# Optimization experiments

Hardware: AMD Instinct MI355X
Metric: run time of the kernel (lower is better)

## Reference

```python
import jax, jax.numpy as jnp
import numpy as np

DIM = 768
HEAD_DIM = 768


def setup_inputs() -> dict:
    key = jax.random.key(0)
    k_x, k_w, k_b = jax.random.split(key, 3)
    x = jax.random.normal(k_x, (4, 4096, DIM), dtype=jnp.float32)
    # torch Linear(dim, 3*head_dim): weight [3H, dim]; store transposed [dim, 3H]
    scale = 1.0 / np.sqrt(DIM)
    W_qkv = jax.random.uniform(k_w, (DIM, 3 * HEAD_DIM), dtype=jnp.float32,
                               minval=-scale, maxval=scale)
    b_qkv = jax.random.uniform(k_b, (3 * HEAD_DIM,), dtype=jnp.float32,
                               minval=-scale, maxval=scale)
    return {"x": x, "W_qkv": W_qkv, "b_qkv": b_qkv}


def reference(x, W_qkv, b_qkv):
    # x: [B, N, C]
    qkv = jnp.einsum("bnc,ch->bnh", x, W_qkv) + b_qkv  # [B, N, 3H]
    q, k, v = jnp.split(qkv, 3, axis=-1)               # each [B, N, H]
    H = q.shape[-1]
    scores = jnp.einsum("bnh,bmh->bnm", q, k) / jnp.sqrt(jnp.float32(H))
    attn = jax.nn.softmax(scores, axis=-1)             # [B, N, N]
    out = jnp.einsum("bnm,bmh->bnh", attn, v)          # [B, N, H]
    return out
```

## Files before the change

### kernel.cpp

```cpp
#include <hip/hip_runtime.h>
#include <stdint.h>

typedef __attribute__((ext_vector_type(8))) short short8;
typedef __attribute__((ext_vector_type(4))) float f32x4;

#define DIM 768
#define H3 2304
#define SEQ 4096
#define NTOK 16384

__device__ __forceinline__ unsigned short f2bf(float f) {
  union { float f; uint32_t u; } c; c.f = f;
  uint32_t u = c.u;
  u += 0x7FFFu + ((u >> 16) & 1u);
  return (unsigned short)(u >> 16);
}

__device__ __forceinline__ void async_cp16(const void* g, void* l) {
  __builtin_amdgcn_global_load_lds(
      (__attribute__((address_space(1))) void*)(void*)g,
      (__attribute__((address_space(3))) void*)l, 16, 0, 0);
}

#define MEMFENCE() asm volatile("" ::: "memory")
#define BARRIER() do { MEMFENCE(); __builtin_amdgcn_s_barrier(); MEMFENCE(); } while (0)
#define WAIT_LGK0() do { asm volatile("s_waitcnt lgkmcnt(0)" ::: "memory"); \
                         __builtin_amdgcn_sched_barrier(0); } while (0)
#define WAIT_VMCNT(n) asm volatile("s_waitcnt vmcnt(" #n ")" ::: "memory")

template<int JN>
__device__ __forceinline__ void gemm_nt64_t(
    const unsigned short* __restrict__ A, const unsigned short* __restrict__ B,
    int K, int ldA, int ldB,
    unsigned short* As, unsigned short* Bs, f32x4 acc[4][JN])
{
  const int tid = threadIdx.x, lane = tid & 63, wid = tid >> 6;
  const int wm = (wid & 1) << 6, wn = (wid >> 1) * (JN * 16);
  const int lr = lane & 15, q = lane >> 4;

#pragma unroll
  for (int i = 0; i < 4; ++i)
#pragma unroll
    for (int j = 0; j < JN; ++j)
      acc[i][j] = (f32x4){0.f, 0.f, 0.f, 0.f};

  const unsigned short* gA[4];
  const unsigned short* gB[JN];
#pragma unroll
  for (int t = 0; t < 4; ++t) {
    const int c = tid + 256 * t;
    const int row = c >> 3, sc = c & 7;
    gA[t] = A + (size_t)row * ldA + (((sc ^ (row & 7)) << 3));
  }
#pragma unroll
  for (int t = 0; t < JN; ++t) {
    const int c = tid + 256 * t;
    const int row = c >> 3, sc = c & 7;
    gB[t] = B + (size_t)row * ldB + (((sc ^ (row & 7)) << 3));
  }

  for (int k0 = 0; k0 < K; k0 += 64) {
#pragma unroll
    for (int t = 0; t < 4; ++t)
      async_cp16(gA[t] + k0, As + (tid + 256 * t) * 8);
#pragma unroll
    for (int t = 0; t < JN; ++t)
      async_cp16(gB[t] + k0, Bs + (tid + 256 * t) * 8);
    __syncthreads();

    short8 af[4][2], bfr[JN][2];
#pragma unroll
    for (int i = 0; i < 4; ++i) {
      const int ra = wm + i * 16 + lr;
#pragma unroll
      for (int s2 = 0; s2 < 2; ++s2)
        af[i][s2] = *(const short8*)(As + ra * 64 + (((s2 * 4 + q) ^ (ra & 7)) << 3));
    }
#pragma unroll
    for (int j = 0; j < JN; ++j) {
      const int rb = wn + j * 16 + lr;
#pragma unroll
      for (int s2 = 0; s2 < 2; ++s2)
        bfr[j][s2] = *(const short8*)(Bs + rb * 64 + (((s2 * 4 + q) ^ (rb & 7)) << 3));
    }
#pragma unroll
    for (int s2 = 0; s2 < 2; ++s2)
#pragma unroll
      for (int i = 0; i < 4; ++i)
#pragma unroll
        for (int j = 0; j < JN; ++j)
          acc[i][j] = __builtin_amdgcn_mfma_f32_16x16x32_bf16(af[i][s2], bfr[j][s2], acc[i][j], 0, 0, 0);
    __syncthreads();
  }
}

template<int JN>
__device__ __forceinline__ void gemm256_nt(
    const unsigned short* __restrict__ A, const unsigned short* __restrict__ B,
    int K, int ldA, int ldB, unsigned short* lds, f32x4 acc[8][JN])
{
  const int tid = threadIdx.x, lane = tid & 63, wid = tid >> 6;
  const int wr = wid >> 2, wc = wid & 3;
  const int lr = lane & 15, q = lane >> 4;

  unsigned short* const As0 = lds;
  unsigned short* const As1 = lds + 16384;
  unsigned short* const Bs0 = lds + 32768;
  unsigned short* const Bs1 = lds + 32768 + JN * 4096;

#pragma unroll
  for (int i = 0; i < 8; ++i)
#pragma unroll
    for (int j = 0; j < JN; ++j)
      acc[i][j] = (f32x4){0.f, 0.f, 0.f, 0.f};

  const unsigned short* gA[4];
  const unsigned short* gB[JN];
#pragma unroll
  for (int t = 0; t < 4; ++t) {
    const int c = tid + 512 * t, row = c >> 3, sc = c & 7;
    gA[t] = A + (size_t)row * ldA + ((sc ^ (row & 7)) << 3);
  }
#pragma unroll
  for (int t = 0; t < JN; ++t) {
    const int c = tid + 512 * t, row = c >> 3, sc = c & 7;
    gB[t] = B + (size_t)row * ldB + ((sc ^ (row & 7)) << 3);
  }

  const int nt = K >> 6;

#pragma unroll
  for (int t = 0; t < 4; ++t) async_cp16(gA[t], As0 + (tid + 512 * t) * 8);
#pragma unroll
  for (int t = 0; t < JN; ++t) async_cp16(gB[t], Bs0 + (tid + 512 * t) * 8);
  const int k1 = (nt > 1) ? 64 : 0;
#pragma unroll
  for (int t = 0; t < 4; ++t) async_cp16(gA[t] + k1, As1 + (tid + 512 * t) * 8);
  WAIT_VMCNT(4);
  BARRIER();

  short8 af[8], bf01[2], bfr[(JN > 2) ? (JN - 2) : 1];

#pragma unroll 2
  for (int t = 0; t < nt; ++t) {
    const int p = t & 1;
    const unsigned short* const Asp = p ? As1 : As0;
    const unsigned short* const Bsp = p ? Bs1 : Bs0;
    unsigned short* const Bsn = p ? Bs0 : Bs1;
    unsigned short* const Asn = p ? As1 : As0;
    const int kB = ((t + 1 < nt) ? t + 1 : nt - 1) << 6;
    const int kA = ((t + 2 < nt) ? t + 2 : nt - 1) << 6;

    async_cp16(gB[0] + kB, Bsn + tid * 8);
    async_cp16(gB[1] + kB, Bsn + (tid + 512) * 8);
#pragma unroll
    for (int i = 0; i < 8; ++i) {
      const int ra = wr * 128 + i * 16 + lr;
      af[i] = *(const short8*)(Asp + ra * 64 + ((q ^ (ra & 7)) << 3));
    }
#pragma unroll
    for (int j = 0; j < 2; ++j) {
      const int rb = wc * (JN * 16) + j * 16 + lr;
      bf01[j] = *(const short8*)(Bsp + rb * 64 + ((q ^ (rb & 7)) << 3));
    }
    BARRIER();
    WAIT_LGK0();
    __builtin_amdgcn_s_setprio(1);
#pragma unroll
    for (int i = 0; i < 8; ++i)
#pragma unroll
      for (int j = 0; j < 2; ++j)
        acc[i][j] = __builtin_amdgcn_mfma_f32_16x16x32_bf16(af[i], bf01[j], acc[i][j], 0, 0, 0);
    __builtin_amdgcn_s_setprio(0);
    BARRIER();

#pragma unroll
    for (int u = 2; u < JN; ++u)
      async_cp16(gB[u] + kB, Bsn + (tid + 512 * u) * 8);
#pragma unroll
    for (int j = 2; j < JN; ++j) {
      const int rb = wc * (JN * 16) + j * 16 + lr;
      bfr[j - 2] = *(const short8*)(Bsp + rb * 64 + ((q ^ (rb & 7)) << 3));
    }
    BARRIER();
    WAIT_LGK0();
    __builtin_amdgcn_s_setprio(1);
#pragma unroll
    for (int i = 0; i < 8; ++i)
#pragma unroll
      for (int j = 2; j < JN; ++j)
        acc[i][j] = __builtin_amdgcn_mfma_f32_16x16x32_bf16(af[i], bfr[j - 2], acc[i][j], 0, 0, 0);
    __builtin_amdgcn_s_setprio(0);
    BARRIER();

#pragma unroll
    for (int i = 0; i < 8; ++i) {
      const int ra = wr * 128 + i * 16 + lr;
      af[i] = *(const short8*)(Asp + ra * 64 + (((4 + q) ^ (ra & 7)) << 3));
    }
#pragma unroll
    for (int j = 0; j < 2; ++j) {
      const int rb = wc * (JN * 16) + j * 16 + lr;
      bf01[j] = *(const short8*)(Bsp + rb * 64 + (((4 + q) ^ (rb & 7)) << 3));
    }
    BARRIER();
    WAIT_LGK0();
    __builtin_amdgcn_s_setprio(1);
#pragma unroll
    for (int i = 0; i < 8; ++i)
#pragma unroll
      for (int j = 0; j < 2; ++j)
        acc[i][j] = __builtin_amdgcn_mfma_f32_16x16x32_bf16(af[i], bf01[j], acc[i][j], 0, 0, 0);
    __builtin_amdgcn_s_setprio(0);
    BARRIER();

#pragma unroll
    for (int u = 0; u < 4; ++u)
      async_cp16(gA[u] + kA, Asn + (tid + 512 * u) * 8);
#pragma unroll
    for (int j = 2; j < JN; ++j) {
      const int rb = wc * (JN * 16) + j * 16 + lr;
      bfr[j - 2] = *(const short8*)(Bsp + rb * 64 + (((4 + q) ^ (rb & 7)) << 3));
    }
    BARRIER();
    WAIT_LGK0();
    __builtin_amdgcn_s_setprio(1);
#pragma unroll
    for (int i = 0; i < 8; ++i)
#pragma unroll
      for (int j = 2; j < JN; ++j)
        acc[i][j] = __builtin_amdgcn_mfma_f32_16x16x32_bf16(af[i], bfr[j - 2], acc[i][j], 0, 0, 0);
    __builtin_amdgcn_s_setprio(0);
    WAIT_VMCNT(4);
    BARRIER();
  }
  WAIT_VMCNT(0);
  BARRIER();
}

__global__ __launch_bounds__(256) void k_cvt(const float* __restrict__ in,
                                             unsigned short* __restrict__ o) {
  int i = blockIdx.x * 256 + threadIdx.x;
  float4 f = ((const float4*)in)[i];
  ushort4 u;
  u.x = f2bf(f.x); u.y = f2bf(f.y); u.z = f2bf(f.z); u.w = f2bf(f.w);
  ((ushort4*)o)[i] = u;
}

__global__ __launch_bounds__(256) void k_transpose(const float* __restrict__ W,
                                                   unsigned short* __restrict__ Wt) {
  __shared__ float tile[32][33];
  const int bc = blockIdx.x * 32;
  const int br = blockIdx.y * 32;
  const int tx = threadIdx.x & 31, ty = threadIdx.x >> 5;
#pragma unroll
  for (int i = 0; i < 32; i += 8)
    tile[ty + i][tx] = W[(size_t)(br + ty + i) * H3 + bc + tx];
  __syncthreads();
#pragma unroll
  for (int i = 0; i < 32; i += 8)
    Wt[(size_t)(bc + ty + i) * DIM + br + tx] = f2bf(tile[tx][ty + i]);
}

__global__ __launch_bounds__(256) void k_qkv(
    const unsigned short* __restrict__ xbf, const unsigned short* __restrict__ Wt,
    const float* __restrict__ bias,
    unsigned short* __restrict__ qb, unsigned short* __restrict__ kb,
    unsigned short* __restrict__ vT)
{
  __shared__ unsigned short As[128 * 64];
  __shared__ unsigned short Bs[128 * 64];
  f32x4 acc[4][4];
  const int g = blockIdx.x;
  const int xcd = g & 7, slot = g >> 3;
  const int tn = slot % 18, grp = slot / 18;
  const int tm = xcd + 8 * grp;
  gemm_nt64_t<4>(xbf + (size_t)(tm * 128) * DIM, Wt + (size_t)(tn * 128) * DIM,
                 DIM, DIM, DIM, As, Bs, acc);

  const int tid = threadIdx.x, lane = tid & 63, wid = tid >> 6;
  const int wm = (wid & 1) << 6, wn = (wid >> 1) << 6;
  const float scale = 0.036084391824351615f;
#pragma unroll
  for (int i = 0; i < 4; ++i) {
#pragma unroll
    for (int j = 0; j < 4; ++j) {
      const int col  = tn * 128 + wn + j * 16 + (lane & 15);
      const int row0 = tm * 128 + wm + i * 16 + ((lane >> 4) << 2);
      const float bc = bias[col];
#pragma unroll
      for (int r = 0; r < 4; ++r) {
        const int row = row0 + r;
        const float v = acc[i][j][r] + bc;
        if (col < 768) {
          qb[(size_t)row * DIM + col] = f2bf(v * scale);
        } else if (col < 1536) {
          kb[(size_t)row * DIM + (col - 768)] = f2bf(v);
        } else {
          const int b = row >> 12, n = row & 4095;
          vT[((size_t)b * DIM + (col - 1536)) * SEQ + n] = f2bf(v);
        }
      }
    }
  }
}

__global__ __launch_bounds__(512, 2) void k_scores(
    const unsigned short* __restrict__ qb, const unsigned short* __restrict__ kb,
    unsigned short* __restrict__ S, float* __restrict__ lpart)
{
  __shared__ unsigned short lds[65536];
  f32x4 acc[8][4];
  const int g = blockIdx.x;
  const int xcd = g & 7, slot = g >> 3;
  const int grp = slot & 7, tn = slot >> 3;
  const int b  = xcd >> 1;
  const int ty = (grp << 1) | (xcd & 1);
  gemm256_nt<4>(qb + ((size_t)b * SEQ + ty * 256) * DIM,
                kb + ((size_t)b * SEQ + tn * 256) * DIM,
                DIM, DIM, DIM, lds, acc);

  const int tid = threadIdx.x, lane = tid & 63, wid = tid >> 6;
  const int wr = wid >> 2, wc = wid & 3;
  const int lr = lane & 15, q = lane >> 4;

  float rs[8][4];
#pragma unroll
  for (int i = 0; i < 8; ++i)
#pragma unroll
    for (int r = 0; r < 4; ++r) rs[i][r] = 0.f;

#pragma unroll
  for (int i = 0; i < 8; ++i)
#pragma unroll
    for (int j = 0; j < 4; ++j) {
      const int col = wc * 64 + j * 16 + lr;
#pragma unroll
      for (int r = 0; r < 4; ++r) {
        const int row = wr * 128 + i * 16 + (q << 2) + r;
        const float e = __expf(acc[i][j][r]);
        lds[row * 256 + (((col >> 3) ^ (((row >> 2) & 3) << 1)) << 3) + (col & 7)] = f2bf(e);
        rs[i][r] += e;
      }
    }

  float* lp = lpart + (size_t)(tn * 4 + wc) * NTOK;
  const int lbase = b * SEQ + ty * 256 + wr * 128 + (q << 2);
#pragma unroll
  for (int i = 0; i < 8; ++i)
#pragma unroll
    for (int r = 0; r < 4; ++r) {
      float v = rs[i][r];
      v += __shfl_xor(v, 1); v += __shfl_xor(v, 2);
      v += __shfl_xor(v, 4); v += __shfl_xor(v, 8);
      if (lr == 0) lp[lbase + i * 16 + r] = v;
    }
  __syncthreads();
  unsigned short* Sb = S + (size_t)b * SEQ * SEQ;
  const int rL = tid >> 5, cc = tid & 31;
#pragma unroll
  for (int pp = 0; pp < 16; ++pp) {
    const int row = pp * 16 + rL;
    const int pos = cc ^ (((row >> 2) & 3) << 1);
    *(uint4*)(Sb + (size_t)(ty * 256 + row) * SEQ + tn * 256 + cc * 8) =
        *(const uint4*)(lds + row * 256 + pos * 8);
  }
}

__global__ __launch_bounds__(256) void k_lred(const float* __restrict__ lpart,
                                              float* __restrict__ lsum) {
  const int tid = threadIdx.x;
  const int row = blockIdx.x * 64 + (tid >> 2);
  const int part = tid & 3;
  float s = 0.f;
#pragma unroll
  for (int t = 0; t < 16; ++t)
    s += lpart[(size_t)(part * 16 + t) * NTOK + row];
  s += __shfl_xor(s, 1);
  s += __shfl_xor(s, 2);
  if (part == 0) lsum[row] = 1.0f / s;
}

__global__ __launch_bounds__(512, 2) void k_pv(
    const unsigned short* __restrict__ P, const unsigned short* __restrict__ vT,
    const float* __restrict__ lsum, float* __restrict__ out)
{
  __shared__ unsigned short lds[57344];
  f32x4 acc[8][3];
  const int g = blockIdx.x;
  const int xcd = g & 7, s = g >> 3;
  const int combo = xcd * 2 + (s & 1);
  const int b = combo >> 2, tn = combo & 3;
  const int tm = s >> 1;
  gemm256_nt<3>(P + (size_t)b * SEQ * SEQ + (size_t)(tm * 256) * SEQ,
                vT + (size_t)b * DIM * SEQ + (size_t)(tn * 192) * SEQ,
                SEQ, SEQ, SEQ, lds, acc);

  const int tid = threadIdx.x, lane = tid & 63, wid = tid >> 6;
  const int wr = wid >> 2, wc = wid & 3;
  const int lr = lane & 15, q = lane >> 4;
  const int lbase = b * SEQ + tm * 256 + wr * 128 + (q << 2);
  float inv[8][4];
#pragma unroll
  for (int i = 0; i < 8; ++i)
#pragma unroll
    for (int r = 0; r < 4; ++r) inv[i][r] = lsum[lbase + i * 16 + r];
  float* ob = out + (size_t)b * SEQ * DIM;
#pragma unroll
  for (int i = 0; i < 8; ++i)
#pragma unroll
    for (int j = 0; j < 3; ++j) {
      const int col  = tn * 192 + wc * 48 + j * 16 + lr;
      const int row0 = tm * 256 + wr * 128 + i * 16 + (q << 2);
#pragma unroll
      for (int r = 0; r < 4; ++r)
        ob[(size_t)(row0 + r) * DIM + col] = acc[i][j][r] * inv[i][r];
    }
}

extern "C" void kernel_launch(void* const* d_in, const int* in_sizes, int n_in,
                              void* d_out, int out_size, void* d_ws, size_t ws_size,
                              hipStream_t stream) {
  const float* x    = (const float*)d_in[0];
  const float* W    = (const float*)d_in[1];
  const float* bias = (const float*)d_in[2];
  float* out = (float*)d_out;

  char* w = (char*)d_ws;
  unsigned short* x_bf = (unsigned short*)(w);
  unsigned short* Wt   = (unsigned short*)(w + 25165824);
  unsigned short* qb   = (unsigned short*)(w + 28704768);
  unsigned short* kb   = (unsigned short*)(w + 53870592);
  unsigned short* vT   = (unsigned short*)(w + 79036416);
  unsigned short* S    = (unsigned short*)(w + 104202240);
  float* lpart = (float*)(w);
  float* lsum  = (float*)(w + 4194304);

  k_cvt      <<<12288, 256, 0, stream>>>(x, x_bf);
  k_transpose<<<dim3(72, 24), 256, 0, stream>>>(W, Wt);
  k_qkv      <<<2304, 256, 0, stream>>>(x_bf, Wt, bias, qb, kb, vT);
  k_scores   <<<1024, 512, 0, stream>>>(qb, kb, S, lpart);
  k_lred     <<<256, 256, 0, stream>>>(lpart, lsum);
  k_pv       <<<256, 512, 0, stream>>>(S, vT, lsum, out);
}
```

Baseline: 426.2 us.

## Pipeline LDS fragment loads with partial lgkmcnt waits and fewer barriers

Restructures the 256-tile GEMM main loop so LDS fragment reads for the next MFMA phase are issued before the current phase, using partial lgkmcnt waits instead of full drains. The per-iteration barrier count drops from about eight to two, and all B tile async copies are issued at loop start. LDS offsets are precomputed outside the loop. This trades higher register pressure (two A fragment sets live at once) for less synchronisation stall and better overlap of LDS reads with MFMA work. The hardcoded lgkmcnt(10) assumes a specific JN.

```diff
diff --git a/kernel.cpp b/kernel.cpp
--- a/kernel.cpp
+++ b/kernel.cpp
@@ -24,9 +24,13 @@
 
 #define MEMFENCE() asm volatile("" ::: "memory")
 #define BARRIER() do { MEMFENCE(); __builtin_amdgcn_s_barrier(); MEMFENCE(); } while (0)
-#define WAIT_LGK0() do { asm volatile("s_waitcnt lgkmcnt(0)" ::: "memory"); \
-                         __builtin_amdgcn_sched_barrier(0); } while (0)
 #define WAIT_VMCNT(n) asm volatile("s_waitcnt vmcnt(" #n ")" ::: "memory")
+
+template <int N>
+__device__ __forceinline__ void wait_lgk() {
+  asm volatile("s_waitcnt lgkmcnt(%0)" :: "n"(N) : "memory");
+  __builtin_amdgcn_sched_barrier(0);
+}
 
 template<int JN>
 __device__ __forceinline__ void gemm_nt64_t(
@@ -99,6 +103,7 @@
     const unsigned short* __restrict__ A, const unsigned short* __restrict__ B,
     int K, int ldA, int ldB, unsigned short* lds, f32x4 acc[8][JN])
 {
+  constexpr int NB = JN - 2;
   const int tid = threadIdx.x, lane = tid & 63, wid = tid >> 6;
   const int wr = wid >> 2, wc = wid & 3;
   const int lr = lane & 15, q = lane >> 4;
@@ -127,6 +132,22 @@
     gB[t] = B + (size_t)row * ldB + ((sc ^ (row & 7)) << 3);
   }
 
+  unsigned offA[8][2], offB[JN][2];
+#pragma unroll
+  for (int i = 0; i < 8; ++i) {
+    const int ra = wr * 128 + i * 16 + lr;
+#pragma unroll
+    for (int h = 0; h < 2; ++h)
+      offA[i][h] = ra * 64 + (((h * 4 + q) ^ (ra & 7)) << 3);
+  }
+#pragma unroll
+  for (int j = 0; j < JN; ++j) {
+    const int rb = wc * (JN * 16) + j * 16 + lr;
+#pragma unroll
+    for (int h = 0; h < 2; ++h)
+      offB[j][h] = rb * 64 + (((h * 4 + q) ^ (rb & 7)) << 3);
+  }
+
   const int nt = K >> 6;
 
 #pragma unroll
@@ -138,8 +159,6 @@
   for (int t = 0; t < 4; ++t) async_cp16(gA[t] + k1, As1 + (tid + 512 * t) * 8);
   WAIT_VMCNT(4);
   BARRIER();
-
-  short8 af[8], bf01[2], bfr[(JN > 2) ? (JN - 2) : 1];
 
 #pragma unroll 2
   for (int t = 0; t < nt; ++t) {
@@ -151,86 +170,67 @@
     const int kB = ((t + 1 < nt) ? t + 1 : nt - 1) << 6;
     const int kA = ((t + 2 < nt) ? t + 2 : nt - 1) << 6;
 
-    async_cp16(gB[0] + kB, Bsn + tid * 8);
-    async_cp16(gB[1] + kB, Bsn + (tid + 512) * 8);
-#pragma unroll
-    for (int i = 0; i < 8; ++i) {
-      const int ra = wr * 128 + i * 16 + lr;
-      af[i] = *(const short8*)(Asp + ra * 64 + ((q ^ (ra & 7)) << 3));
-    }
-#pragma unroll
-    for (int j = 0; j < 2; ++j) {
-      const int rb = wc * (JN * 16) + j * 16 + lr;
-      bf01[j] = *(const short8*)(Bsp + rb * 64 + ((q ^ (rb & 7)) << 3));
-    }
+#pragma unroll
+    for (int u = 0; u < JN; ++u)
+      async_cp16(gB[u] + kB, Bsn + (tid + 512 * u) * 8);
+
+    short8 fa0[8], fa1[8], fbj[2], fbk[(NB > 0) ? NB : 1];
+#pragma unroll
+    for (int i = 0; i < 8; ++i) fa0[i] = *(const short8*)(Asp + offA[i][0]);
+#pragma unroll
+    for (int j = 0; j < 2; ++j) fbj[j] = *(const short8*)(Bsp + offB[j][0]);
+#pragma unroll
+    for (int j = 0; j < NB; ++j) fbk[j] = *(const short8*)(Bsp + offB[2 + j][0]);
+
+    wait_lgk<NB>();
+    __builtin_amdgcn_s_setprio(1);
+#pragma unroll
+    for (int i = 0; i < 8; ++i)
+#pragma unroll
+      for (int j = 0; j < 2; ++j)
+        acc[i][j] = __builtin_amdgcn_mfma_f32_16x16x32_bf16(fa0[i], fbj[j], acc[i][j], 0, 0, 0);
+    __builtin_amdgcn_s_setprio(0);
+
+#pragma unroll
+    for (int i = 0; i < 8; ++i) fa1[i] = *(const short8*)(Asp + offA[i][1]);
+#pragma unroll
+    for (int j = 0; j < 2; ++j) fbj[j] = *(const short8*)(Bsp + offB[j][1]);
+
+    wait_lgk<10>();
+    __builtin_amdgcn_s_setprio(1);
+#pragma unroll
+    for (int i = 0; i < 8; ++i)
+#pragma unroll
+      for (int j = 0; j < NB; ++j)
+        acc[i][2 + j] = __builtin_amdgcn_mfma_f32_16x16x32_bf16(fa0[i], fbk[j], acc[i][2 + j], 0, 0, 0);
+    __builtin_amdgcn_s_setprio(0);
+
+#pragma unroll
+    for (int j = 0; j < NB; ++j) fbk[j] = *(const short8*)(Bsp + offB[2 + j][1]);
+
+    wait_lgk<NB>();
+    __builtin_amdgcn_s_setprio(1);
+#pragma unroll
+    for (int i = 0; i < 8; ++i)
+#pragma unroll
+      for (int j = 0; j < 2; ++j)
+        acc[i][j] = __builtin_amdgcn_mfma_f32_16x16x32_bf16(fa1[i], fbj[j], acc[i][j], 0, 0, 0);
+    __builtin_amdgcn_s_setprio(0);
+
     BARRIER();
-    WAIT_LGK0();
-    __builtin_amdgcn_s_setprio(1);
-#pragma unroll
-    for (int i = 0; i < 8; ++i)
-#pragma unroll
-      for (int j = 0; j < 2; ++j)
-        acc[i][j] = __builtin_amdgcn_mfma_f32_16x16x32_bf16(af[i], bf01[j], acc[i][j], 0, 0, 0);
-    __builtin_amdgcn_s_setprio(0);
-    BARRIER();
-
-#pragma unroll
-    for (int u = 2; u < JN; ++u)
-      async_cp16(gB[u] + kB, Bsn + (tid + 512 * u) * 8);
-#pragma unroll
-    for (int j = 2; j < JN; ++j) {
-      const int rb = wc * (JN * 16) + j * 16 + lr;
-      bfr[j - 2] = *(const short8*)(Bsp + rb * 64 + ((q ^ (rb & 7)) << 3));
-    }
-    BARRIER();
-    WAIT_LGK0();
-    __builtin_amdgcn_s_setprio(1);
-#pragma unroll
-    for (int i = 0; i < 8; ++i)
-#pragma unroll
-      for (int j = 2; j < JN; ++j)
-        acc[i][j] = __builtin_amdgcn_mfma_f32_16x16x32_bf16(af[i], bfr[j - 2], acc[i][j], 0, 0, 0);
-    __builtin_amdgcn_s_setprio(0);
-    BARRIER();
-
-#pragma unroll
-    for (int i = 0; i < 8; ++i) {
-      const int ra = wr * 128 + i * 16 + lr;
-      af[i] = *(const short8*)(Asp + ra * 64 + (((4 + q) ^ (ra & 7)) << 3));
-    }
-#pragma unroll
-    for (int j = 0; j < 2; ++j) {
-      const int rb = wc * (JN * 16) + j * 16 + lr;
-      bf01[j] = *(const short8*)(Bsp + rb * 64 + (((4 + q) ^ (rb & 7)) << 3));
-    }
-    BARRIER();
-    WAIT_LGK0();
-    __builtin_amdgcn_s_setprio(1);
-#pragma unroll
-    for (int i = 0; i < 8; ++i)
-#pragma unroll
-      for (int j = 0; j < 2; ++j)
-        acc[i][j] = __builtin_amdgcn_mfma_f32_16x16x32_bf16(af[i], bf01[j], acc[i][j], 0, 0, 0);
-    __builtin_amdgcn_s_setprio(0);
-    BARRIER();
-
 #pragma unroll
     for (int u = 0; u < 4; ++u)
       async_cp16(gA[u] + kA, Asn + (tid + 512 * u) * 8);
-#pragma unroll
-    for (int j = 2; j < JN; ++j) {
-      const int rb = wc * (JN * 16) + j * 16 + lr;
-      bfr[j - 2] = *(const short8*)(Bsp + rb * 64 + (((4 + q) ^ (rb & 7)) << 3));
-    }
-    BARRIER();
-    WAIT_LGK0();
+
+    wait_lgk<0>();
     __builtin_amdgcn_s_setprio(1);
 #pragma unroll
     for (int i = 0; i < 8; ++i)
 #pragma unroll
-      for (int j = 2; j < JN; ++j)
-        acc[i][j] = __builtin_amdgcn_mfma_f32_16x16x32_bf16(af[i], bfr[j - 2], acc[i][j], 0, 0, 0);
+      for (int j = 0; j < NB; ++j)
+        acc[i][2 + j] = __builtin_amdgcn_mfma_f32_16x16x32_bf16(fa1[i], fbk[j], acc[i][2 + j], 0, 0, 0);
     __builtin_amdgcn_s_setprio(0);
+
     WAIT_VMCNT(4);
     BARRIER();
   }
```

Result: no change. 422.0 us, median of 2 (-1.0%).
